# Performance work log

Hardware: AMD Instinct MI355X
Metric: run time of the kernel (lower is better)

Reference implementation:

```python
import jax, jax.numpy as jnp
import numpy as np

NUM_EMB = 1024
EMB_DIM = 256
COMMITMENT_COST = 0.25


def setup_inputs() -> dict:
    key = jax.random.key(0)
    k1, k2 = jax.random.split(key)
    inp = jax.random.normal(k1, (64, EMB_DIM, 32, 32), dtype=jnp.float32)  # [B, C, H, W]
    emb_weight = jax.random.uniform(
        k2, (NUM_EMB, EMB_DIM), minval=-1.0 / NUM_EMB, maxval=1.0 / NUM_EMB, dtype=jnp.float32
    )
    return {"inp": inp, "emb_weight": emb_weight}


def reference(inp, emb_weight):
    sg = jax.lax.stop_gradient
    x = jnp.transpose(inp, (0, 2, 3, 1))              # [B, H, W, C]
    flat = x.reshape(-1, EMB_DIM)                      # [N, C]
    d = (jnp.sum(flat * flat, axis=1, keepdims=True)
         + jnp.sum(emb_weight * emb_weight, axis=1)
         - 2.0 * (flat @ emb_weight.T))
    idx = jnp.argmin(d, axis=1)                        # [N]
    encodings = jax.nn.one_hot(idx, NUM_EMB, dtype=jnp.float32)  # [N, K]
    e = emb_weight[idx].reshape(x.shape)               # [B, H, W, C]
    loss = jnp.mean((e - sg(x)) ** 2) + COMMITMENT_COST * jnp.mean((sg(e) - x) ** 2)
    e_ste = x + sg(e - x)                              # straight-through estimator
    avg_probs = jnp.mean(encodings, axis=0)
    perplexity = jnp.exp(-jnp.sum(avg_probs * jnp.log(avg_probs + 1e-10)))
    out = jnp.transpose(e_ste, (0, 3, 1, 2))           # back to [B, C, H, W]
    return loss, out, perplexity, encodings
```

## Files before the change

### kernel.cpp

```cpp
#include <hip/hip_runtime.h>
#include <hip/hip_bf16.h>
#include <math.h>
#include <float.h>

#define BB    64
#define CCH   256
#define KKE   1024
#define HWN   1024
#define NTOT  (BB*HWN)
#define OUT_ELE (BB*CCH*HWN)
#define LOSS_OFF 0
#define OUT_OFF  1
#define PERP_OFF (1 + OUT_ELE)
#define ENC_OFF  (2 + OUT_ELE)

#define WS_IDX    0
#define WS_ANORM  262144
#define WS_HIST   524288
#define WS_BNORM  528384
#define WS_MISC   532480
#define WS_LIST   536576
#define WS_EMBT   798720
#define WS_EHI    1847296
#define WS_ELO    2371584
#define WS_CD1    2895872
#define WS_CK1    4993024
#define WS_CD2    7090176
#define WS_AHI    9187328
#define WS_ALO    42741760

typedef __attribute__((ext_vector_type(4))) float f32x4;
typedef __attribute__((ext_vector_type(8))) short s16x8;

#define TAU 2e-4f
#define RB  8

__device__ __forceinline__ void gload16(const short* g, void* l) {
    __builtin_amdgcn_global_load_lds(
        (const __attribute__((address_space(1))) unsigned int*)g,
        (__attribute__((address_space(3))) unsigned int*)l,
        16, 0, 0);
}

__device__ inline void merge_cand(float& d1, int& k1, float& d2,
                                  float od1, int ok1, float od2) {
    bool w = (od1 < d1) || (od1 == d1 && ok1 < k1);
    float loser_d1 = w ? d1 : od1;
    float winner_d2 = w ? od2 : d2;
    d2 = fminf(winner_d2, loser_d1);
    if (w) { d1 = od1; k1 = ok1; }
}

__global__ __launch_bounds__(256) void prep_kernel(const float* __restrict__ emb,
                                                   float* __restrict__ embT,
                                                   float* __restrict__ bnorm,
                                                   short* __restrict__ ehi,
                                                   short* __restrict__ elo,
                                                   unsigned int* __restrict__ hist,
                                                   float* __restrict__ misc) {
    const int k = blockIdx.x;
    const int t = threadIdx.x;
    float v = emb[k*CCH + t];
    embT[(size_t)t*KKE + k] = v;
    __hip_bfloat16 h = __float2bfloat16(v);
    float hf = __bfloat162float(h);
    __hip_bfloat16 l = __float2bfloat16(v - hf);
    const int u  = (t & 31) >> 3;
    const int sw = (k >> 1) & 3;
    size_t eoff = (size_t)(t >> 5)*32768 + (size_t)k*32 + (size_t)((u ^ sw)*8 + (t & 7));
    ehi[eoff] = *(short*)&h;
    elo[eoff] = *(short*)&l;
    double sq = (double)v * (double)v;
    #pragma unroll
    for (int off = 32; off; off >>= 1) sq += __shfl_down(sq, off);
    __shared__ double wred[4];
    const int wave = t >> 6, lane = t & 63;
    if (lane == 0) wred[wave] = sq;
    __syncthreads();
    if (t == 0) bnorm[k] = (float)(wred[0] + wred[1] + wred[2] + wred[3]);
    if (blockIdx.x < 4) hist[blockIdx.x*256 + t] = 0u;
    if (blockIdx.x == 4 && t == 0) { misc[0] = 0.0f; ((int*)misc)[1] = 0; }
}

__global__ __launch_bounds__(256) void asplit_kernel(const float* __restrict__ inp,
                                                     short* __restrict__ ahi,
                                                     short* __restrict__ alo,
                                                     float* __restrict__ anorm) {
    __shared__ short th[256*32];
    __shared__ short tl[256*32];
    const int t  = threadIdx.x;
    const int b  = blockIdx.y;
    const int hw = blockIdx.x * 256 + t;
    const int n  = b * HWN + hw;
    const int n0 = b * HWN + blockIdx.x * 256;
    const float* src = inp + (size_t)b*CCH*HWN + hw;
    const int sw = (t >> 1) & 3;
    double s = 0.0;
    for (int chunk = 0; chunk < 8; ++chunk) {
        s16x8 hs[4], ls[4];
        #pragma unroll
        for (int cc = 0; cc < 32; ++cc) {
            float v = src[(size_t)(chunk*32 + cc)*HWN];
            s += (double)v * (double)v;
            __hip_bfloat16 h = __float2bfloat16(v);
            float hf = __bfloat162float(h);
            __hip_bfloat16 l = __float2bfloat16(v - hf);
            hs[cc >> 3][cc & 7] = *(short*)&h;
            ls[cc >> 3][cc & 7] = *(short*)&l;
        }
        __syncthreads();
        #pragma unroll
        for (int u = 0; u < 4; ++u) {
            *(s16x8*)&th[t*32 + ((u ^ sw) << 3)] = hs[u];
            *(s16x8*)&tl[t*32 + ((u ^ sw) << 3)] = ls[u];
        }
        __syncthreads();
        const size_t obase = ((size_t)chunk*NTOT + (size_t)n0) * 32;
        #pragma unroll
        for (int i = 0; i < 4; ++i) {
            const int so = i*2048 + t*8;
            *(s16x8*)&ahi[obase + so] = *(const s16x8*)&th[so];
            *(s16x8*)&alo[obase + so] = *(const s16x8*)&tl[so];
        }
    }
    anorm[n] = (float)s;
}

__global__ __launch_bounds__(256, 3) void argmin_mfma(const short* __restrict__ ahi,
                                                      const short* __restrict__ alo,
                                                      const short* __restrict__ ehi,
                                                      const short* __restrict__ elo,
                                                      const float* __restrict__ anorm,
                                                      const float* __restrict__ bnorm,
                                                      float* __restrict__ cd1,
                                                      int* __restrict__ ck1,
                                                      float* __restrict__ cd2) {
    __shared__ short smem[4][4096];

    const int t    = threadIdx.x;
    const int w    = t >> 6;
    const int lane = t & 63;
    const int q    = lane >> 4;
    const int l15  = lane & 15;
    const int L    = blockIdx.x;
    const int bx   = (L & 7) + ((L >> 6) << 3);
    const int by   = (L >> 3) & 7;
    const int n0   = bx * 128;
    const int k0   = by * 128;

    f32x4 acc[2][8];
    #pragma unroll
    for (int i = 0; i < 2; ++i)
        #pragma unroll
        for (int j = 0; j < 8; ++j) acc[i][j] = (f32x4){0.f,0.f,0.f,0.f};

    const int swu = (q ^ ((l15 >> 1) & 3)) << 4;
    const int ra0 = (w*32 + l15)*64 + swu;

    for (int chunk = 0; chunk < 8; ++chunk) {
        __syncthreads();
        {
            const short* as = ahi + (size_t)chunk*2097152 + (size_t)n0*32;
            const short* al = alo + (size_t)chunk*2097152 + (size_t)n0*32;
            const short* bs = ehi + (size_t)chunk*32768  + (size_t)k0*32;
            const short* bl = elo + (size_t)chunk*32768  + (size_t)k0*32;
            #pragma unroll
            for (int i = 0; i < 2; ++i) {
                const size_t so = (size_t)i*2048 + (size_t)t*8;
                const int    lo = i*4096 + w*1024;
                gload16(as + so, (char*)&smem[0][0] + lo);
                gload16(al + so, (char*)&smem[1][0] + lo);
                gload16(bs + so, (char*)&smem[2][0] + lo);
                gload16(bl + so, (char*)&smem[3][0] + lo);
            }
        }
        __syncthreads();
        const char* LAh = (const char*)&smem[0][0];
        const char* LAl = (const char*)&smem[1][0];
        const char* LBh = (const char*)&smem[2][0];
        const char* LBl = (const char*)&smem[3][0];
        s16x8 afh0 = *(const s16x8*)(LAh + ra0);
        s16x8 afh1 = *(const s16x8*)(LAh + ra0 + 1024);
        s16x8 afl0 = *(const s16x8*)(LAl + ra0);
        s16x8 afl1 = *(const s16x8*)(LAl + ra0 + 1024);
        #pragma unroll
        for (int ct = 0; ct < 8; ++ct) {
            const int rb = (ct*16 + l15)*64 + swu;
            s16x8 bh = *(const s16x8*)(LBh + rb);
            s16x8 bl = *(const s16x8*)(LBl + rb);
            acc[0][ct] = __builtin_amdgcn_mfma_f32_16x16x32_bf16(afh0, bh, acc[0][ct], 0, 0, 0);
            acc[0][ct] = __builtin_amdgcn_mfma_f32_16x16x32_bf16(afh0, bl, acc[0][ct], 0, 0, 0);
            acc[0][ct] = __builtin_amdgcn_mfma_f32_16x16x32_bf16(afl0, bh, acc[0][ct], 0, 0, 0);
            acc[1][ct] = __builtin_amdgcn_mfma_f32_16x16x32_bf16(afh1, bh, acc[1][ct], 0, 0, 0);
            acc[1][ct] = __builtin_amdgcn_mfma_f32_16x16x32_bf16(afh1, bl, acc[1][ct], 0, 0, 0);
            acc[1][ct] = __builtin_amdgcn_mfma_f32_16x16x32_bf16(afl1, bh, acc[1][ct], 0, 0, 0);
        }
    }

    float bnv[8];
    #pragma unroll
    for (int ct = 0; ct < 8; ++ct) bnv[ct] = bnorm[k0 + ct*16 + l15];

    #pragma unroll
    for (int rg = 0; rg < 2; ++rg) {
        #pragma unroll
        for (int reg = 0; reg < 4; ++reg) {
            const int n = n0 + w*32 + rg*16 + q*4 + reg;
            const float a = anorm[n];
            float d1 = FLT_MAX, d2 = FLT_MAX; int k1 = 0;
            #pragma unroll
            for (int ct = 0; ct < 8; ++ct) {
                float s = a + bnv[ct];
                float d = s - 2.0f * acc[rg][ct][reg];
                int   k = k0 + ct*16 + l15;
                if (d < d1 || (d == d1 && k < k1)) { d2 = d1; d1 = d; k1 = k; }
                else d2 = fminf(d2, d);
            }
            #pragma unroll
            for (int off = 1; off < 16; off <<= 1) {
                float od1 = __shfl_xor(d1, off);
                int   ok1 = __shfl_xor(k1, off);
                float od2 = __shfl_xor(d2, off);
                merge_cand(d1, k1, d2, od1, ok1, od2);
            }
            if (l15 == 0) {
                const size_t o = (size_t)by*NTOT + n;
                cd1[o] = d1; ck1[o] = k1; cd2[o] = d2;
            }
        }
    }
}

__global__ __launch_bounds__(256) void reduce_kernel(const float* __restrict__ cd1,
                                                     const int* __restrict__ ck1,
                                                     const float* __restrict__ cd2,
                                                     int* __restrict__ idx,
                                                     int* __restrict__ list,
                                                     int* __restrict__ counter) {
    const int n = blockIdx.x*256 + threadIdx.x;
    float d1 = cd1[n]; int k1 = ck1[n]; float d2 = cd2[n];
    #pragma unroll
    for (int kb = 1; kb < 8; ++kb) {
        const size_t o = (size_t)kb*NTOT + n;
        merge_cand(d1, k1, d2, cd1[o], ck1[o], cd2[o]);
    }
    idx[n] = k1;
    if (d2 - d1 < TAU) {
        int p = atomicAdd(counter, 1);
        list[p] = n;
    }
}

__global__ __launch_bounds__(256) void rescore_kernel(const float* __restrict__ inp,
                                                      const float* __restrict__ embT,
                                                      const float* __restrict__ anorm,
                                                      const float* __restrict__ bnorm,
                                                      const int* __restrict__ list,
                                                      const int* __restrict__ counter,
                                                      int* __restrict__ idx) {
    __shared__ float xs[RB][256];
    __shared__ float wd[RB][4];
    __shared__ int   wk[RB][4];
    __shared__ int   ls[RB];
    const int t = threadIdx.x;
    const int wave = t >> 6, lane = t & 63;
    const int cnt = *counter;
    const int ngrp = (cnt + RB - 1) / RB;
    float bn[4];
    #pragma unroll
    for (int kk = 0; kk < 4; ++kk) bn[kk] = bnorm[kk*256 + t];

    for (int g = blockIdx.x; g < ngrp; g += gridDim.x) {
        const int base = g * RB;
        const int m = min(RB, cnt - base);
        __syncthreads();
        if (t < RB) ls[t] = list[base + ((t < m) ? t : 0)];
        __syncthreads();
        #pragma unroll
        for (int j = 0; j < RB; ++j) {
            const int n = ls[j];
            xs[j][t] = inp[(size_t)(n >> 10)*CCH*HWN + (size_t)t*HWN + (n & 1023)];
        }
        __syncthreads();
        float dots[RB][4];
        #pragma unroll
        for (int j = 0; j < RB; ++j)
            #pragma unroll
            for (int kk = 0; kk < 4; ++kk) dots[j][kk] = 0.f;
        #pragma unroll 4
        for (int c = 0; c < CCH; ++c) {
            const float* row = embT + (size_t)c*KKE + t;
            const float e0 = row[0], e1 = row[256], e2 = row[512], e3 = row[768];
            #pragma unroll
            for (int j = 0; j < RB; ++j) {
                const float xc = xs[j][c];
                dots[j][0] += xc * e0;
                dots[j][1] += xc * e1;
                dots[j][2] += xc * e2;
                dots[j][3] += xc * e3;
            }
        }
        #pragma unroll
        for (int j = 0; j < RB; ++j) {
            const float a = anorm[ls[j]];
            float bd = FLT_MAX; int bk = 0;
            #pragma unroll
            for (int kk = 0; kk < 4; ++kk) {
                const int k = kk*256 + t;
                float s = a + bn[kk];
                float d = s - 2.0f * dots[j][kk];
                if (d < bd || (d == bd && k < bk)) { bd = d; bk = k; }
            }
            #pragma unroll
            for (int off = 1; off < 64; off <<= 1) {
                float od = __shfl_xor(bd, off);
                int   ok = __shfl_xor(bk, off);
                if (od < bd || (od == bd && ok < bk)) { bd = od; bk = ok; }
            }
            if (lane == 0) { wd[j][wave] = bd; wk[j][wave] = bk; }
        }
        __syncthreads();
        if (t < m) {
            float bd = wd[t][0]; int bk = wk[t][0];
            #pragma unroll
            for (int wv = 1; wv < 4; ++wv) {
                float od = wd[t][wv]; int ok = wk[t][wv];
                if (od < bd || (od == bd && ok < bk)) { bd = od; bk = ok; }
            }
            idx[ls[t]] = bk;
        }
    }
}

#define ENC_BLK 2048
#define OL_BLK  4096
__global__ __launch_bounds__(256) void tail_kernel(const float* __restrict__ inp,
                                                   const float* __restrict__ embT,
                                                   const int* __restrict__ idx,
                                                   float* __restrict__ enc,
                                                   float* __restrict__ out,
                                                   unsigned int* __restrict__ hist,
                                                   float* __restrict__ lossacc) {
    const int t = threadIdx.x;
    if (blockIdx.x < ENC_BLK) {
        const int n0 = blockIdx.x * 32;
        int kr[32];
        #pragma unroll
        for (int r4 = 0; r4 < 8; ++r4) {
            int4 kv = *(const int4*)&idx[n0 + r4*4];
            kr[r4*4+0] = kv.x; kr[r4*4+1] = kv.y; kr[r4*4+2] = kv.z; kr[r4*4+3] = kv.w;
        }
        const int j4 = t*4 + 2;
        #pragma unroll 8
        for (int r = 0; r < 32; ++r) {
            const int k = kr[r];
            float* row = enc + (size_t)(n0 + r) * KKE;
            if (t < 255) {
                float4 v = {0.f,0.f,0.f,0.f};
                if (k == j4)     v.x = 1.f;
                if (k == j4 + 1) v.y = 1.f;
                if (k == j4 + 2) v.z = 1.f;
                if (k == j4 + 3) v.w = 1.f;
                *(float4*)&row[j4] = v;
            } else {
                float2 h  = {0.f,0.f}, tl = {0.f,0.f};
                if (k == 0)    h.x  = 1.f;
                if (k == 1)    h.y  = 1.f;
                if (k == 1022) tl.x = 1.f;
                if (k == 1023) tl.y = 1.f;
                *(float2*)&row[0]    = h;
                *(float2*)&row[1022] = tl;
            }
            if (t == 0) atomicAdd(&hist[k], 1u);
        }
    } else {
        const size_t stride = (size_t)OL_BLK * 256;
        float lsum = 0.0f;
        for (size_t m = (size_t)(blockIdx.x - ENC_BLK) * 256 + t; m < (size_t)OUT_ELE; m += stride) {
            int hw = (int)(m & 1023);
            int c  = (int)((m >> 10) & 255);
            int b  = (int)(m >> 18);
            int k  = idx[b*HWN + hw];
            float e = embT[(size_t)c*KKE + k];
            float x = inp[m];
            out[m] = e;
            float df = e - x;
            lsum += df * df;
        }
        #pragma unroll
        for (int off = 32; off; off >>= 1) lsum += __shfl_down(lsum, off);
        __shared__ float wred[4];
        const int wave = t >> 6, lane = t & 63;
        if (lane == 0) wred[wave] = lsum;
        __syncthreads();
        if (t == 0) atomicAdd(lossacc, wred[0] + wred[1] + wred[2] + wred[3]);
    }
}

__global__ __launch_bounds__(1024) void final_kernel(const unsigned int* __restrict__ hist,
                                                     const float* __restrict__ lossacc,
                                                     float* __restrict__ d_out) {
    const int t = threadIdx.x;
    float p = (float)hist[t] * (1.0f / 65536.0f);
    float v = p * logf(p + 1e-10f);
    #pragma unroll
    for (int off = 32; off; off >>= 1) v += __shfl_down(v, off);
    __shared__ float wred[16];
    const int wave = t >> 6, lane = t & 63;
    if (lane == 0) wred[wave] = v;
    __syncthreads();
    if (t == 0) {
        float s = 0.0f;
        #pragma unroll
        for (int i = 0; i < 16; ++i) s += wred[i];
        d_out[PERP_OFF] = expf(-s);
        d_out[LOSS_OFF] = 1.25f * (*lossacc) * (1.0f / (float)OUT_ELE);
    }
}

extern "C" void kernel_launch(void* const* d_in, const int* in_sizes, int n_in,
                              void* d_out, int out_size, void* d_ws, size_t ws_size,
                              hipStream_t stream) {
    (void)in_sizes; (void)n_in; (void)out_size; (void)ws_size;
    const float* inp = (const float*)d_in[0];
    const float* emb = (const float*)d_in[1];
    float* out = (float*)d_out;
    char* ws = (char*)d_ws;
    int*          idx     = (int*)(ws + WS_IDX);
    float*        anorm   = (float*)(ws + WS_ANORM);
    unsigned int* hist    = (unsigned int*)(ws + WS_HIST);
    float*        bnorm   = (float*)(ws + WS_BNORM);
    float*        misc    = (float*)(ws + WS_MISC);
    int*          list    = (int*)(ws + WS_LIST);
    float*        embT    = (float*)(ws + WS_EMBT);
    short*        ehi     = (short*)(ws + WS_EHI);
    short*        elo     = (short*)(ws + WS_ELO);
    float*        cd1     = (float*)(ws + WS_CD1);
    int*          ck1     = (int*)(ws + WS_CK1);
    float*        cd2     = (float*)(ws + WS_CD2);
    short*        ahi     = (short*)(ws + WS_AHI);
    short*        alo     = (short*)(ws + WS_ALO);
    int*          counter = ((int*)misc) + 1;

    prep_kernel<<<dim3(KKE), dim3(256), 0, stream>>>(emb, embT, bnorm, ehi, elo, hist, misc);
    asplit_kernel<<<dim3(4, BB), dim3(256), 0, stream>>>(inp, ahi, alo, anorm);
    argmin_mfma<<<dim3(4096), dim3(256), 0, stream>>>(ahi, alo, ehi, elo, anorm, bnorm, cd1, ck1, cd2);
    reduce_kernel<<<dim3(256), dim3(256), 0, stream>>>(cd1, ck1, cd2, idx, list, counter);
    rescore_kernel<<<dim3(512), dim3(256), 0, stream>>>(inp, embT, anorm, bnorm, list, counter, idx);
    tail_kernel<<<dim3(ENC_BLK + OL_BLK), dim3(256), 0, stream>>>(inp, embT, idx, out + ENC_OFF, out + OUT_OFF, hist, misc);
    final_kernel<<<dim3(1), dim3(1024), 0, stream>>>(hist, misc, out);
}
```

Measured before the change: 633.7 us.

## Merge prep and split kernels, use nontemporal stores, retune occupancy and tail grid

Fuses the codebook prep and input split into one launch, which removes a launch and lets the two independent jobs run side by side. The one-hot encoding and output writes now use nontemporal stores, so these large streaming writes should pollute the cache less. It also doubles the encoding block count with fewer rows per block, and raises the argmin kernel's launch-bounds occupancy hint from 3 to 4, which may force register spilling.

```diff
diff --git a/kernel.cpp b/kernel.cpp
--- a/kernel.cpp
+++ b/kernel.cpp
@@ -30,6 +30,7 @@
 #define WS_ALO    42741760
 
 typedef __attribute__((ext_vector_type(4))) float f32x4;
+typedef __attribute__((ext_vector_type(2))) float f32x2;
 typedef __attribute__((ext_vector_type(8))) short s16x8;
 
 #define TAU 2e-4f
@@ -51,82 +52,83 @@
     if (w) { d1 = od1; k1 = ok1; }
 }
 
-__global__ __launch_bounds__(256) void prep_kernel(const float* __restrict__ emb,
-                                                   float* __restrict__ embT,
-                                                   float* __restrict__ bnorm,
-                                                   short* __restrict__ ehi,
-                                                   short* __restrict__ elo,
-                                                   unsigned int* __restrict__ hist,
-                                                   float* __restrict__ misc) {
-    const int k = blockIdx.x;
+__global__ __launch_bounds__(256) void prep_split_kernel(const float* __restrict__ emb,
+                                                         float* __restrict__ embT,
+                                                         float* __restrict__ bnorm,
+                                                         short* __restrict__ ehi,
+                                                         short* __restrict__ elo,
+                                                         unsigned int* __restrict__ hist,
+                                                         float* __restrict__ misc,
+                                                         const float* __restrict__ inp,
+                                                         short* __restrict__ ahi,
+                                                         short* __restrict__ alo,
+                                                         float* __restrict__ anorm) {
     const int t = threadIdx.x;
-    float v = emb[k*CCH + t];
-    embT[(size_t)t*KKE + k] = v;
-    __hip_bfloat16 h = __float2bfloat16(v);
-    float hf = __bfloat162float(h);
-    __hip_bfloat16 l = __float2bfloat16(v - hf);
-    const int u  = (t & 31) >> 3;
-    const int sw = (k >> 1) & 3;
-    size_t eoff = (size_t)(t >> 5)*32768 + (size_t)k*32 + (size_t)((u ^ sw)*8 + (t & 7));
-    ehi[eoff] = *(short*)&h;
-    elo[eoff] = *(short*)&l;
-    double sq = (double)v * (double)v;
-    #pragma unroll
-    for (int off = 32; off; off >>= 1) sq += __shfl_down(sq, off);
-    __shared__ double wred[4];
-    const int wave = t >> 6, lane = t & 63;
-    if (lane == 0) wred[wave] = sq;
-    __syncthreads();
-    if (t == 0) bnorm[k] = (float)(wred[0] + wred[1] + wred[2] + wred[3]);
-    if (blockIdx.x < 4) hist[blockIdx.x*256 + t] = 0u;
-    if (blockIdx.x == 4 && t == 0) { misc[0] = 0.0f; ((int*)misc)[1] = 0; }
-}
-
-__global__ __launch_bounds__(256) void asplit_kernel(const float* __restrict__ inp,
-                                                     short* __restrict__ ahi,
-                                                     short* __restrict__ alo,
-                                                     float* __restrict__ anorm) {
-    __shared__ short th[256*32];
-    __shared__ short tl[256*32];
-    const int t  = threadIdx.x;
-    const int b  = blockIdx.y;
-    const int hw = blockIdx.x * 256 + t;
-    const int n  = b * HWN + hw;
-    const int n0 = b * HWN + blockIdx.x * 256;
-    const float* src = inp + (size_t)b*CCH*HWN + hw;
-    const int sw = (t >> 1) & 3;
-    double s = 0.0;
-    for (int chunk = 0; chunk < 8; ++chunk) {
-        s16x8 hs[4], ls[4];
-        #pragma unroll
-        for (int cc = 0; cc < 32; ++cc) {
-            float v = src[(size_t)(chunk*32 + cc)*HWN];
-            s += (double)v * (double)v;
-            __hip_bfloat16 h = __float2bfloat16(v);
-            float hf = __bfloat162float(h);
-            __hip_bfloat16 l = __float2bfloat16(v - hf);
-            hs[cc >> 3][cc & 7] = *(short*)&h;
-            ls[cc >> 3][cc & 7] = *(short*)&l;
-        }
-        __syncthreads();
-        #pragma unroll
-        for (int u = 0; u < 4; ++u) {
-            *(s16x8*)&th[t*32 + ((u ^ sw) << 3)] = hs[u];
-            *(s16x8*)&tl[t*32 + ((u ^ sw) << 3)] = ls[u];
-        }
-        __syncthreads();
-        const size_t obase = ((size_t)chunk*NTOT + (size_t)n0) * 32;
-        #pragma unroll
-        for (int i = 0; i < 4; ++i) {
-            const int so = i*2048 + t*8;
-            *(s16x8*)&ahi[obase + so] = *(const s16x8*)&th[so];
-            *(s16x8*)&alo[obase + so] = *(const s16x8*)&tl[so];
-        }
-    }
-    anorm[n] = (float)s;
-}
-
-__global__ __launch_bounds__(256, 3) void argmin_mfma(const short* __restrict__ ahi,
+    if (blockIdx.x < KKE) {
+        const int k = blockIdx.x;
+        float v = emb[k*CCH + t];
+        embT[(size_t)t*KKE + k] = v;
+        __hip_bfloat16 h = __float2bfloat16(v);
+        float hf = __bfloat162float(h);
+        __hip_bfloat16 l = __float2bfloat16(v - hf);
+        const int u  = (t & 31) >> 3;
+        const int sw = (k >> 1) & 3;
+        size_t eoff = (size_t)(t >> 5)*32768 + (size_t)k*32 + (size_t)((u ^ sw)*8 + (t & 7));
+        ehi[eoff] = *(short*)&h;
+        elo[eoff] = *(short*)&l;
+        double sq = (double)v * (double)v;
+        #pragma unroll
+        for (int off = 32; off; off >>= 1) sq += __shfl_down(sq, off);
+        __shared__ double wred[4];
+        const int wave = t >> 6, lane = t & 63;
+        if (lane == 0) wred[wave] = sq;
+        __syncthreads();
+        if (t == 0) bnorm[k] = (float)(wred[0] + wred[1] + wred[2] + wred[3]);
+        if (blockIdx.x < 4) hist[blockIdx.x*256 + t] = 0u;
+        if (blockIdx.x == 4 && t == 0) { misc[0] = 0.0f; ((int*)misc)[1] = 0; }
+    } else {
+        __shared__ short th[256*32];
+        __shared__ short tl[256*32];
+        const int id = blockIdx.x - KKE;
+        const int b  = id >> 2;
+        const int hw = (id & 3) * 256 + t;
+        const int n  = b * HWN + hw;
+        const int n0 = n - t;
+        const float* src = inp + (size_t)b*CCH*HWN + hw;
+        const int sw = (t >> 1) & 3;
+        double s = 0.0;
+        for (int chunk = 0; chunk < 8; ++chunk) {
+            s16x8 hs[4], ls[4];
+            #pragma unroll
+            for (int cc = 0; cc < 32; ++cc) {
+                float v = src[(size_t)(chunk*32 + cc)*HWN];
+                s += (double)v * (double)v;
+                __hip_bfloat16 h = __float2bfloat16(v);
+                float hf = __bfloat162float(h);
+                __hip_bfloat16 l = __float2bfloat16(v - hf);
+                hs[cc >> 3][cc & 7] = *(short*)&h;
+                ls[cc >> 3][cc & 7] = *(short*)&l;
+            }
+            __syncthreads();
+            #pragma unroll
+            for (int u = 0; u < 4; ++u) {
+                *(s16x8*)&th[t*32 + ((u ^ sw) << 3)] = hs[u];
+                *(s16x8*)&tl[t*32 + ((u ^ sw) << 3)] = ls[u];
+            }
+            __syncthreads();
+            const size_t obase = ((size_t)chunk*NTOT + (size_t)n0) * 32;
+            #pragma unroll
+            for (int i = 0; i < 4; ++i) {
+                const int so = i*2048 + t*8;
+                *(s16x8*)&ahi[obase + so] = *(const s16x8*)&th[so];
+                *(s16x8*)&alo[obase + so] = *(const s16x8*)&tl[so];
+            }
+        }
+        anorm[n] = (float)s;
+    }
+}
+
+__global__ __launch_bounds__(256, 4) void argmin_mfma(const short* __restrict__ ahi,
                                                       const short* __restrict__ alo,
                                                       const short* __restrict__ ehi,
                                                       const short* __restrict__ elo,
@@ -332,7 +334,7 @@
     }
 }
 
-#define ENC_BLK 2048
+#define ENC_BLK 4096
 #define OL_BLK  4096
 __global__ __launch_bounds__(256) void tail_kernel(const float* __restrict__ inp,
                                                    const float* __restrict__ embT,
@@ -343,33 +345,33 @@
                                                    float* __restrict__ lossacc) {
     const int t = threadIdx.x;
     if (blockIdx.x < ENC_BLK) {
-        const int n0 = blockIdx.x * 32;
-        int kr[32];
-        #pragma unroll
-        for (int r4 = 0; r4 < 8; ++r4) {
+        const int n0 = blockIdx.x * 16;
+        int kr[16];
+        #pragma unroll
+        for (int r4 = 0; r4 < 4; ++r4) {
             int4 kv = *(const int4*)&idx[n0 + r4*4];
             kr[r4*4+0] = kv.x; kr[r4*4+1] = kv.y; kr[r4*4+2] = kv.z; kr[r4*4+3] = kv.w;
         }
         const int j4 = t*4 + 2;
         #pragma unroll 8
-        for (int r = 0; r < 32; ++r) {
+        for (int r = 0; r < 16; ++r) {
             const int k = kr[r];
             float* row = enc + (size_t)(n0 + r) * KKE;
             if (t < 255) {
-                float4 v = {0.f,0.f,0.f,0.f};
+                f32x4 v = {0.f,0.f,0.f,0.f};
                 if (k == j4)     v.x = 1.f;
                 if (k == j4 + 1) v.y = 1.f;
                 if (k == j4 + 2) v.z = 1.f;
                 if (k == j4 + 3) v.w = 1.f;
-                *(float4*)&row[j4] = v;
+                __builtin_nontemporal_store(v, (f32x4*)&row[j4]);
             } else {
-                float2 h  = {0.f,0.f}, tl = {0.f,0.f};
+                f32x2 h  = {0.f,0.f}, tl = {0.f,0.f};
                 if (k == 0)    h.x  = 1.f;
                 if (k == 1)    h.y  = 1.f;
                 if (k == 1022) tl.x = 1.f;
                 if (k == 1023) tl.y = 1.f;
-                *(float2*)&row[0]    = h;
-                *(float2*)&row[1022] = tl;
+                __builtin_nontemporal_store(h,  (f32x2*)&row[0]);
+                __builtin_nontemporal_store(tl, (f32x2*)&row[1022]);
             }
             if (t == 0) atomicAdd(&hist[k], 1u);
         }
@@ -383,7 +385,7 @@
             int k  = idx[b*HWN + hw];
             float e = embT[(size_t)c*KKE + k];
             float x = inp[m];
-            out[m] = e;
+            __builtin_nontemporal_store(e, &out[m]);
             float df = e - x;
             lsum += df * df;
         }
@@ -442,8 +444,8 @@
     short*        alo     = (short*)(ws + WS_ALO);
     int*          counter = ((int*)misc) + 1;
 
-    prep_kernel<<<dim3(KKE), dim3(256), 0, stream>>>(emb, embT, bnorm, ehi, elo, hist, misc);
-    asplit_kernel<<<dim3(4, BB), dim3(256), 0, stream>>>(inp, ahi, alo, anorm);
+    prep_split_kernel<<<dim3(KKE + 256), dim3(256), 0, stream>>>(emb, embT, bnorm, ehi, elo,
+                                                                 hist, misc, inp, ahi, alo, anorm);
     argmin_mfma<<<dim3(4096), dim3(256), 0, stream>>>(ahi, alo, ehi, elo, anorm, bnorm, cd1, ck1, cd2);
     reduce_kernel<<<dim3(256), dim3(256), 0, stream>>>(cd1, ck1, cd2, idx, list, counter);
     rescore_kernel<<<dim3(512), dim3(256), 0, stream>>>(inp, embT, anorm, bnorm, list, counter, idx);
```

Result: slower. 647.5 us (+2.2%).
